# Performance work log

Hardware: AMD Instinct MI355X
Metric: run time of the kernel (lower is better)

## Reference

```python
import jax, jax.numpy as jnp
import numpy as np

B, N, D, H = 2, 4096, 512, 8
DH = D // H
FF = 4 * D
SCALE = D ** (-0.5)  # standard_scale=False -> dim**-0.5
EPS = 1e-5


def layernorm(x, w, b):
    mu = jnp.mean(x, axis=-1, keepdims=True)
    var = jnp.mean(jnp.square(x - mu), axis=-1, keepdims=True)
    return (x - mu) * jax.lax.rsqrt(var + EPS) * w + b


def setup_inputs() -> dict:
    key = jax.random.key(0)
    ks = jax.random.split(key, 12)
    s = lambda fin: 1.0 / np.sqrt(fin)
    return {
        "x": jax.random.normal(ks[0], (B, N, D), jnp.float32),
        "gamma": jax.random.uniform(ks[1], (B,), jnp.float32),
        "dist": jax.random.uniform(ks[2], (N, N), jnp.float32),
        "ln1_w": jnp.ones((D,), jnp.float32),
        "ln1_b": jnp.zeros((D,), jnp.float32),
        "qkv_w": jax.random.normal(ks[3], (D, 3 * D), jnp.float32) * s(D),
        "qkv_b": jnp.zeros((3 * D,), jnp.float32),
        "proj_w": jax.random.normal(ks[4], (D, D), jnp.float32) * s(D),
        "proj_b": jnp.zeros((D,), jnp.float32),
        "ln2_w": jnp.ones((D,), jnp.float32),
        "ln2_b": jnp.zeros((D,), jnp.float32),
        "fc1_w": jax.random.normal(ks[5], (D, FF), jnp.float32) * s(D),
        "fc1_b": jnp.zeros((FF,), jnp.float32),
        "fc2_w": jax.random.normal(ks[6], (FF, D), jnp.float32) * s(FF),
        "fc2_b": jnp.zeros((D,), jnp.float32),
    }


def reference(x, gamma, dist, ln1_w, ln1_b, qkv_w, qkv_b, proj_w, proj_b,
              ln2_w, ln2_b, fc1_w, fc1_b, fc2_w, fc2_b):
    # --- attention branch ---
    h = layernorm(x, ln1_w, ln1_b)                       # [B,N,D]
    qkv = h @ qkv_w + qkv_b                              # [B,N,3D]
    qkv = qkv.reshape(B, N, 3, H, DH).transpose(2, 0, 3, 1, 4)  # [3,B,H,N,DH]
    q, k, v = qkv[0], qkv[1], qkv[2]
    scores = jnp.einsum('bhnd,bhmd->bhnm', q, k) * SCALE
    scores = scores - gamma[:, None, None, None] * dist[None, None]
    w = jax.nn.softmax(scores, axis=-1)                  # [B,H,N,N]
    out = jnp.einsum('bhnm,bhmd->bhnd', w, v)            # [B,H,N,DH]
    out = out.transpose(0, 2, 1, 3).reshape(B, N, D)
    x = x + out @ proj_w + proj_b
    # --- MLP branch ---
    h = layernorm(x, ln2_w, ln2_b)
    h = jax.nn.gelu(h @ fc1_w + fc1_b, approximate=False)
    x = x + h @ fc2_w + fc2_b
    return x
```

## Files before the change

kernel.cpp:

```cpp
#include <hip/hip_runtime.h>
#include <math.h>

typedef __bf16 bf16x8 __attribute__((ext_vector_type(8)));
typedef __bf16 bf16x4 __attribute__((ext_vector_type(4)));
typedef float  f32x4  __attribute__((ext_vector_type(4)));
typedef unsigned int u32x4 __attribute__((ext_vector_type(4)));

#define B_   2
#define N_   4096
#define D_   512
#define H_   8
#define FF_  2048
#define BN_  (B_*N_)
static constexpr float SCALE_ = 0.04419417382415922f;
static constexpr float LOG2E_ = 1.44269504088896341f;
static constexpr float SCALE_L2E_ = SCALE_ * LOG2E_;

#define GLOAD_LDS16(g, l) __builtin_amdgcn_global_load_lds( \
    (const __attribute__((address_space(1))) void*)(g),     \
    (__attribute__((address_space(3))) void*)(l), 16, 0, 0)

__global__ void transpose_to_bf16(const float* __restrict__ in, __bf16* __restrict__ out,
                                  int R, int C) {
    __shared__ float tile[32][33];
    const int c0 = blockIdx.x * 32, r0 = blockIdx.y * 32;
    const int tx = threadIdx.x, ty = threadIdx.y;
#pragma unroll
    for (int i = 0; i < 4; ++i)
        tile[ty + 8*i][tx] = in[(size_t)(r0 + ty + 8*i) * C + c0 + tx];
    __syncthreads();
#pragma unroll
    for (int i = 0; i < 4; ++i)
        out[(size_t)(c0 + ty + 8*i) * R + r0 + tx] = (__bf16)tile[tx][ty + 8*i];
}

__global__ void cvt_bf16(const float* __restrict__ in, __bf16* __restrict__ out, int n4) {
    int i = blockIdx.x * blockDim.x + threadIdx.x;
    const int stride = gridDim.x * blockDim.x;
    for (; i < n4; i += stride) {
        float4 v = ((const float4*)in)[i];
        bf16x4 o;
        o[0] = (__bf16)(v.x * LOG2E_); o[1] = (__bf16)(v.y * LOG2E_);
        o[2] = (__bf16)(v.z * LOG2E_); o[3] = (__bf16)(v.w * LOG2E_);
        ((bf16x4*)out)[i] = o;
    }
}

__global__ __launch_bounds__(128)
void ln_kernel(const float* __restrict__ x, const float* __restrict__ w,
               const float* __restrict__ b, __bf16* __restrict__ out) {
    const int row = blockIdx.x, t = threadIdx.x;
    const float4 v = *(const float4*)&x[(size_t)row * 512 + t * 4];
    float s  = v.x + v.y + v.z + v.w;
    float sq = v.x*v.x + v.y*v.y + v.z*v.z + v.w*v.w;
#pragma unroll
    for (int mk = 1; mk < 64; mk <<= 1) { s += __shfl_xor(s, mk); sq += __shfl_xor(sq, mk); }
    __shared__ float ps[2][2];
    if ((t & 63) == 0) { ps[t >> 6][0] = s; ps[t >> 6][1] = sq; }
    __syncthreads();
    s = ps[0][0] + ps[1][0]; sq = ps[0][1] + ps[1][1];
    const float mu  = s * (1.0f / 512.0f);
    const float var = sq * (1.0f / 512.0f) - mu * mu;
    const float rs  = rsqrtf(var + 1e-5f);
    const float4 wv = *(const float4*)&w[t * 4];
    const float4 bv = *(const float4*)&b[t * 4];
    bf16x4 o;
    o[0] = (__bf16)((v.x - mu) * rs * wv.x + bv.x);
    o[1] = (__bf16)((v.y - mu) * rs * wv.y + bv.y);
    o[2] = (__bf16)((v.z - mu) * rs * wv.z + bv.z);
    o[3] = (__bf16)((v.w - mu) * rs * wv.w + bv.w);
    *(bf16x4*)&out[(size_t)row * 512 + t * 4] = o;
}

template<int EPI, int BNT, bool DBUF>
__global__ __launch_bounds__(256, 4)
void gemm_bt(const __bf16* __restrict__ A, const __bf16* __restrict__ Bt,
             const float* __restrict__ bias, const float* __restrict__ resid,
             __bf16* __restrict__ outb, float* __restrict__ outf,
             int M, int N, int K) {
    constexpr int NI = BNT / 32;
    constexpr int NB = DBUF ? 2 : 1;
    __shared__ __align__(16) __bf16 As[NB][128 * 64];
    __shared__ __align__(16) __bf16 Bs[NB][BNT * 64];
    const int tid = threadIdx.x;
    const int w = tid >> 6, l = tid & 63;
    const int g = l >> 4, c = l & 15;
    const int m0 = blockIdx.y * 128, n0 = blockIdx.x * BNT;
    const int wm = (w >> 1) * 64, wn = (w & 1) * (BNT / 2);
    f32x4 acc[4][NI] = {};

    auto stage = [&](int kt, int buf) {
#pragma unroll
        for (int i = 0; i < 4; ++i) {
            const int cb = (i * 4 + w) * 64;
            const int chunk = cb + l;
            const int row = chunk >> 3, c8 = chunk & 7;
            GLOAD_LDS16(A + (size_t)(m0 + row) * K + kt + c8 * 8, As[buf] + cb * 8);
        }
#pragma unroll
        for (int i = 0; i < BNT / 32; ++i) {
            const int cb = (i * 4 + w) * 64;
            const int chunk = cb + l;
            const int row = chunk >> 3, c8 = chunk & 7;
            GLOAD_LDS16(Bt + (size_t)(n0 + row) * K + kt + c8 * 8, Bs[buf] + cb * 8);
        }
    };
    auto compute = [&](int buf) {
#pragma unroll
        for (int kk = 0; kk < 2; ++kk) {
            bf16x8 av[4], bv[NI];
#pragma unroll
            for (int mi = 0; mi < 4; ++mi)
                av[mi] = *(const bf16x8*)&As[buf][(wm + mi * 16 + c) * 64 + kk * 32 + g * 8];
#pragma unroll
            for (int ni = 0; ni < NI; ++ni)
                bv[ni] = *(const bf16x8*)&Bs[buf][(wn + ni * 16 + c) * 64 + kk * 32 + g * 8];
#pragma unroll
            for (int mi = 0; mi < 4; ++mi)
#pragma unroll
                for (int ni = 0; ni < NI; ++ni)
                    acc[mi][ni] = __builtin_amdgcn_mfma_f32_16x16x32_bf16(
                        av[mi], bv[ni], acc[mi][ni], 0, 0, 0);
        }
    };

    if constexpr (DBUF) {
        stage(0, 0);
        const int T = K / 64;
        for (int t = 0; t < T; ++t) {
            const int cur = t & 1;
            __syncthreads();
            if (t + 1 < T) stage((t + 1) * 64, cur ^ 1);
            compute(cur);
        }
    } else {
        for (int kt = 0; kt < K; kt += 64) {
            __syncthreads();
            stage(kt, 0);
            __syncthreads();
            compute(0);
        }
    }

    __syncthreads();
    if constexpr (EPI == 2) {
        constexpr int LDW = NI * 16 + 4;
        float* ep = (float*)&As[0][0] + w * (16 * LDW);
#pragma unroll
        for (int mi = 0; mi < 4; ++mi) {
#pragma unroll
            for (int ni = 0; ni < NI; ++ni)
#pragma unroll
                for (int r = 0; r < 4; ++r)
                    ep[(g * 4 + r) * LDW + ni * 16 + c] =
                        acc[mi][ni][r] + bias[n0 + wn + ni * 16 + c];
#pragma unroll
            for (int rnd = 0; rnd < NI; ++rnd) {
                const int idx = rnd * 64 + l;
                const int rr = idx >> 3, cc = idx & 7;
                const f32x4 vv = *(const f32x4*)&ep[rr * LDW + cc * 4];
                const size_t oidx = (size_t)(m0 + wm + mi * 16 + rr) * N + n0 + wn + cc * 4;
                const f32x4 rv = *(const f32x4*)&resid[oidx];
                *(f32x4*)&outf[oidx] = vv + rv;
            }
        }
    } else {
        constexpr int LDW = NI * 16 + 8;
        __bf16* ep = &As[0][0] + w * (16 * LDW);
#pragma unroll
        for (int mi = 0; mi < 4; ++mi) {
#pragma unroll
            for (int ni = 0; ni < NI; ++ni)
#pragma unroll
                for (int r = 0; r < 4; ++r) {
                    float v = acc[mi][ni][r] + bias[n0 + wn + ni * 16 + c];
                    if constexpr (EPI == 1)
                        v = 0.5f * v * (1.0f + erff(v * 0.70710678118654752f));
                    ep[(g * 4 + r) * LDW + ni * 16 + c] = (__bf16)v;
                }
#pragma unroll
            for (int rnd = 0; rnd < NI / 2; ++rnd) {
                const int idx = rnd * 64 + l;
                const int rr = idx >> 3, cc = idx & 7;
                const bf16x8 vv = *(const bf16x8*)&ep[rr * LDW + cc * 8];
                const size_t oidx = (size_t)(m0 + wm + mi * 16 + rr) * N + n0 + wn + cc * 8;
                *(bf16x8*)&outb[oidx] = vv;
            }
        }
    }
}

__global__ __launch_bounds__(512, 4)
void attn_kernel(const __bf16* __restrict__ qkv, const __bf16* __restrict__ distb,
                 const float* __restrict__ gamma, __bf16* __restrict__ outp) {
    __shared__ __align__(16) __bf16 Ks [64 * 64];
    __shared__ __align__(16) __bf16 Vts[64][72];
    __shared__ __align__(16) __bf16 DPs[2][128 * 64];
    const int tid = threadIdx.x;
    const int w = tid >> 6, l = tid & 63;
    const int g = l >> 4, c = l & 15;
    const int wq = w & 3, hn = w >> 2;
    const int qt = blockIdx.x, h = blockIdx.y;
    const int b = blockIdx.z;
    const float gb = gamma[b];
    const size_t tok0 = (size_t)b * N_;
    const int qrow = 16 * wq + c;
    const int wub = tid & 448;
    const int srow = tid >> 3;
    const int sd0  = (tid & 7) * 8;
    const int cswz = ((tid & 7) ^ (srow & 7)) * 8;
    const int swz  = (c & 7) << 3;

    bf16x8 qf[2][2];
#pragma unroll
    for (int t = 0; t < 2; ++t) {
        const size_t qbase = (tok0 + qt * 128 + 64 * t + qrow) * 1536 + h * 64;
#pragma unroll
        for (int kk = 0; kk < 2; ++kk) {
            const bf16x8 qv = *(const bf16x8*)&qkv[qbase + kk * 32 + g * 8];
#pragma unroll
            for (int j = 0; j < 8; ++j) qf[t][kk][j] = (__bf16)((float)qv[j] * SCALE_L2E_);
        }
    }
    bf16x8 ones;
#pragma unroll
    for (int j = 0; j < 8; ++j) ones[j] = (__bf16)1.0f;

    f32x4 acc[2][4] = {};
    f32x4 accl[2] = {};
    bf16x8 vreg;

    const size_t kvstep = (size_t)64 * 1536;
    const __bf16* gk = qkv + 512  + (tok0 + srow) * 1536 + h * 64 + cswz;
    const __bf16* gv = qkv + 1024 + (tok0 + srow) * 1536 + h * 64 + sd0;
    const __bf16* gd = distb + (size_t)(qt * 128 + srow) * N_ + cswz;

    auto issue_k = [&]() {
        GLOAD_LDS16(gk, Ks + wub * 8);
        gk += kvstep;
    };
    auto issue_d = [&](int buf) {
        GLOAD_LDS16(gd,                    DPs[buf] + wub * 8);
        GLOAD_LDS16(gd + (size_t)64 * N_,  DPs[buf] + (512 + wub) * 8);
        gd += 64;
    };
    auto issue_v = [&]() {
        vreg = *(const bf16x8*)gv;
        gv += kvstep;
    };
    auto write_vts = [&]() {
        const int kp = srow ^ sd0;
#pragma unroll
        for (int j = 0; j < 8; ++j) Vts[sd0 + j][kp] = vreg[j];
    };

    const int ktend = N_ / 64;
    issue_k();
    issue_v();
    issue_d(0);

    for (int kt = 0; kt < ktend; ++kt) {
        const int cur = kt & 1;
        __syncthreads();
        write_vts();
        if (kt + 1 < ktend) {
            issue_v();
            issue_d(cur ^ 1);
        }
        __builtin_amdgcn_sched_barrier(0);

        uint32_t W[2][2][2];
#pragma unroll
        for (int nii = 0; nii < 2; ++nii) {
            const int ni = 2 * hn + nii;
            f32x4 s0, s1;
            {
                const bf16x4 dd0 = *(const bf16x4*)
                    &DPs[cur][(qrow << 6) + ((16 * ni + 4 * g) ^ swz)];
                const bf16x4 dd1 = *(const bf16x4*)
                    &DPs[cur][((64 + qrow) << 6) + ((16 * ni + 4 * g) ^ swz)];
#pragma unroll
                for (int r = 0; r < 4; ++r) {
                    s0[r] = -gb * (float)dd0[r];
                    s1[r] = -gb * (float)dd1[r];
                }
            }
            __builtin_amdgcn_s_setprio(1);
#pragma unroll
            for (int kk = 0; kk < 2; ++kk) {
                const bf16x8 kf = *(const bf16x8*)
                    &Ks[((16 * ni + c) << 6) + ((kk * 32 + g * 8) ^ swz)];
                s0 = __builtin_amdgcn_mfma_f32_16x16x32_bf16(kf, qf[0][kk], s0, 0, 0, 0);
                s1 = __builtin_amdgcn_mfma_f32_16x16x32_bf16(kf, qf[1][kk], s1, 0, 0, 0);
            }
            __builtin_amdgcn_s_setprio(0);
#pragma unroll
            for (int t = 0; t < 2; ++t) {
                const f32x4 sv = (t == 0) ? s0 : s1;
                float pv0, pv1, pv2, pv3;
                pv0 = __builtin_amdgcn_exp2f(sv[0]);
                pv1 = __builtin_amdgcn_exp2f(sv[1]);
                pv2 = __builtin_amdgcn_exp2f(sv[2]);
                pv3 = __builtin_amdgcn_exp2f(sv[3]);
                asm("v_cvt_pk_bf16_f32 %0, %1, %2" : "=v"(W[t][nii][0]) : "v"(pv0), "v"(pv1));
                asm("v_cvt_pk_bf16_f32 %0, %1, %2" : "=v"(W[t][nii][1]) : "v"(pv2), "v"(pv3));
            }
        }
        bf16x8 pa[2];
#pragma unroll
        for (int t = 0; t < 2; ++t) {
#pragma unroll
            for (int p = 0; p < 2; ++p) {
                asm("v_permlane32_swap_b32 %0, %1"
                    : "+v"(W[t][0][p]), "+v"(W[t][1][p]));
                asm("v_permlane16_swap_b32 %0, %1"
                    : "+v"(W[t][0][p]), "+v"(W[t][1][p]));
            }
            const u32x4 words = {W[t][0][0], W[t][0][1], W[t][1][0], W[t][1][1]};
            pa[t] = __builtin_bit_cast(bf16x8, words);
        }
        __builtin_amdgcn_sched_barrier(0);
        asm volatile("s_waitcnt lgkmcnt(0)\n\ts_barrier" ::: "memory");
        __builtin_amdgcn_sched_barrier(0);
        if (kt + 1 < ktend) issue_k();

        __builtin_amdgcn_s_setprio(1);
        accl[0] = __builtin_amdgcn_mfma_f32_16x16x32_bf16(ones, pa[0], accl[0], 0, 0, 0);
        accl[1] = __builtin_amdgcn_mfma_f32_16x16x32_bf16(ones, pa[1], accl[1], 0, 0, 0);
#pragma unroll
        for (int di = 0; di < 4; ++di) {
            const int d = 16 * di + c;
            const int kp = (hn * 32 + g * 8) ^ ((d >> 3) << 3);
            const bf16x8 vb = *(const bf16x8*)&Vts[d][kp];
            acc[0][di] = __builtin_amdgcn_mfma_f32_16x16x32_bf16(vb, pa[0], acc[0][di], 0, 0, 0);
            acc[1][di] = __builtin_amdgcn_mfma_f32_16x16x32_bf16(vb, pa[1], acc[1][di], 0, 0, 0);
        }
        __builtin_amdgcn_s_setprio(0);
    }

    __syncthreads();
    float* sacc = (float*)&DPs[0][0];
    float* sl   = (float*)&Ks[0];
    const int slot = wq * 64 + l;
    if (hn == 0) {
#pragma unroll
        for (int t = 0; t < 2; ++t) {
            sl[slot * 2 + t] = accl[t][0];
#pragma unroll
            for (int di = 0; di < 4; ++di)
                *(f32x4*)&sacc[(slot * 8 + t * 4 + di) * 4] = acc[t][di];
        }
    }
    __syncthreads();
    if (hn == 1) {
#pragma unroll
        for (int t = 0; t < 2; ++t) {
            const float rl = 1.0f / (accl[t][0] + sl[slot * 2 + t]);
            const int q = qt * 128 + 64 * t + qrow;
#pragma unroll
            for (int di = 0; di < 4; ++di) {
                const f32x4 oa = acc[t][di] + *(const f32x4*)&sacc[(slot * 8 + t * 4 + di) * 4];
                bf16x4 o;
#pragma unroll
                for (int r = 0; r < 4; ++r) o[r] = (__bf16)(oa[r] * rl);
                *(bf16x4*)&outp[((size_t)(b * N_ + q)) * 512 + h * 64 + 16 * di + 4 * g] = o;
            }
        }
    }
}

extern "C" void kernel_launch(void* const* d_in, const int* in_sizes, int n_in,
                              void* d_out, int out_size, void* d_ws, size_t ws_size,
                              hipStream_t stream) {
    (void)in_sizes; (void)n_in; (void)out_size; (void)ws_size;
    const float* x      = (const float*)d_in[0];
    const float* gamma  = (const float*)d_in[1];
    const float* dist   = (const float*)d_in[2];
    const float* ln1_w  = (const float*)d_in[3];
    const float* ln1_b  = (const float*)d_in[4];
    const float* qkv_w  = (const float*)d_in[5];
    const float* qkv_b  = (const float*)d_in[6];
    const float* proj_w = (const float*)d_in[7];
    const float* proj_b = (const float*)d_in[8];
    const float* ln2_w  = (const float*)d_in[9];
    const float* ln2_b  = (const float*)d_in[10];
    const float* fc1_w  = (const float*)d_in[11];
    const float* fc1_b  = (const float*)d_in[12];
    const float* fc2_w  = (const float*)d_in[13];
    const float* fc2_b  = (const float*)d_in[14];
    float* out = (float*)d_out;

    char* ws = (char*)d_ws;
    size_t off = 0;
    auto alloc = [&](size_t bytes) {
        void* p = ws + off; off = (off + bytes + 255) & ~(size_t)255; return p;
    };
    __bf16* distbf  = (__bf16*)alloc((size_t)N_ * N_ * 2);
    __bf16* qkv_wt  = (__bf16*)alloc((size_t)1536 * 512 * 2);
    __bf16* proj_wt = (__bf16*)alloc((size_t)512 * 512 * 2);
    __bf16* fc1_wt  = (__bf16*)alloc((size_t)2048 * 512 * 2);
    __bf16* fc2_wt  = (__bf16*)alloc((size_t)512 * 2048 * 2);
    __bf16* hbuf    = (__bf16*)alloc((size_t)BN_ * 512 * 2);
    __bf16* qkvbuf  = (__bf16*)alloc((size_t)BN_ * 1536 * 2);
    __bf16* attnbuf = (__bf16*)alloc((size_t)BN_ * 512 * 2);
    float*  x1buf   = (float*) alloc((size_t)BN_ * 512 * 4);
    __bf16* h2buf   = (__bf16*)alloc((size_t)BN_ * 512 * 2);
    __bf16* ffbuf   = (__bf16*)alloc((size_t)BN_ * 2048 * 2);

    const dim3 tb(32, 8);
    transpose_to_bf16<<<dim3(1536/32,  512/32), tb, 0, stream>>>(qkv_w,  qkv_wt,  512, 1536);
    transpose_to_bf16<<<dim3( 512/32,  512/32), tb, 0, stream>>>(proj_w, proj_wt, 512,  512);
    transpose_to_bf16<<<dim3(2048/32,  512/32), tb, 0, stream>>>(fc1_w,  fc1_wt,  512, 2048);
    transpose_to_bf16<<<dim3( 512/32, 2048/32), tb, 0, stream>>>(fc2_w,  fc2_wt, 2048,  512);
    cvt_bf16<<<2048, 256, 0, stream>>>(dist, distbf, N_ * N_ / 4);

    ln_kernel<<<BN_, 128, 0, stream>>>(x, ln1_w, ln1_b, hbuf);
    gemm_bt<0,128,false><<<dim3(1536/128, BN_/128), 256, 0, stream>>>(
        hbuf, qkv_wt, qkv_b, nullptr, qkvbuf, nullptr, BN_, 1536, 512);
    attn_kernel<<<dim3(32, 8, 2), 512, 0, stream>>>(qkvbuf, distbf, gamma, attnbuf);
    gemm_bt<2,64,false><<<dim3(512/64, BN_/128), 256, 0, stream>>>(
        attnbuf, proj_wt, proj_b, x, nullptr, x1buf, BN_, 512, 512);
    ln_kernel<<<BN_, 128, 0, stream>>>(x1buf, ln2_w, ln2_b, h2buf);
    gemm_bt<1,128,false><<<dim3(2048/128, BN_/128), 256, 0, stream>>>(
        h2buf, fc1_wt, fc1_b, nullptr, ffbuf, nullptr, BN_, 2048, 512);
    gemm_bt<2,64,false><<<dim3(512/64, BN_/128), 256, 0, stream>>>(
        ffbuf, fc2_wt, fc2_b, x1buf, nullptr, out, BN_, 512, 2048);
}
```

Measured before the change: 262.3 us.

## Read fp32 distance matrix directly in attention, drop bf16 conversion pre-pass

Removes the separate cvt_bf16 kernel that wrote a bf16 copy of the 4096x4096 distance matrix, so the attention kernel now streams fp32 dist tiles straight into LDS and folds log2e into gamma. The LDS dist tile becomes a single fp32 buffer instead of a double-buffered bf16 one, and its load is moved to after the mid-iteration barrier, next to the K load. This saves a full read-and-write pass over dist but doubles the dist bytes each attention block reads (32 q-tiles x 16 heads re-read it) and drops the double buffering, so dist latency may be less hidden.

```diff
diff --git a/kernel.cpp b/kernel.cpp
--- a/kernel.cpp
+++ b/kernel.cpp
@@ -32,18 +32,6 @@
 #pragma unroll
     for (int i = 0; i < 4; ++i)
         out[(size_t)(c0 + ty + 8*i) * R + r0 + tx] = (__bf16)tile[tx][ty + 8*i];
-}
-
-__global__ void cvt_bf16(const float* __restrict__ in, __bf16* __restrict__ out, int n4) {
-    int i = blockIdx.x * blockDim.x + threadIdx.x;
-    const int stride = gridDim.x * blockDim.x;
-    for (; i < n4; i += stride) {
-        float4 v = ((const float4*)in)[i];
-        bf16x4 o;
-        o[0] = (__bf16)(v.x * LOG2E_); o[1] = (__bf16)(v.y * LOG2E_);
-        o[2] = (__bf16)(v.z * LOG2E_); o[3] = (__bf16)(v.w * LOG2E_);
-        ((bf16x4*)out)[i] = o;
-    }
 }
 
 __global__ __launch_bounds__(128)
@@ -191,18 +179,18 @@
 }
 
 __global__ __launch_bounds__(512, 4)
-void attn_kernel(const __bf16* __restrict__ qkv, const __bf16* __restrict__ distb,
+void attn_kernel(const __bf16* __restrict__ qkv, const float* __restrict__ dist,
                  const float* __restrict__ gamma, __bf16* __restrict__ outp) {
     __shared__ __align__(16) __bf16 Ks [64 * 64];
     __shared__ __align__(16) __bf16 Vts[64][72];
-    __shared__ __align__(16) __bf16 DPs[2][128 * 64];
+    __shared__ __align__(16) float  DPsF[128 * 64];
     const int tid = threadIdx.x;
     const int w = tid >> 6, l = tid & 63;
     const int g = l >> 4, c = l & 15;
     const int wq = w & 3, hn = w >> 2;
     const int qt = blockIdx.x, h = blockIdx.y;
     const int b = blockIdx.z;
-    const float gb = gamma[b];
+    const float gbl = gamma[b] * LOG2E_;
     const size_t tok0 = (size_t)b * N_;
     const int qrow = 16 * wq + c;
     const int wub = tid & 448;
@@ -233,15 +221,18 @@
     const size_t kvstep = (size_t)64 * 1536;
     const __bf16* gk = qkv + 512  + (tok0 + srow) * 1536 + h * 64 + cswz;
     const __bf16* gv = qkv + 1024 + (tok0 + srow) * 1536 + h * 64 + sd0;
-    const __bf16* gd = distb + (size_t)(qt * 128 + srow) * N_ + cswz;
+    const int drow = tid >> 4;
+    const float* gd = dist + (size_t)(qt * 128 + drow) * N_
+                    + ((tid & 15) ^ (drow & 7)) * 4;
 
     auto issue_k = [&]() {
         GLOAD_LDS16(gk, Ks + wub * 8);
         gk += kvstep;
     };
-    auto issue_d = [&](int buf) {
-        GLOAD_LDS16(gd,                    DPs[buf] + wub * 8);
-        GLOAD_LDS16(gd + (size_t)64 * N_,  DPs[buf] + (512 + wub) * 8);
+    auto issue_d = [&]() {
+#pragma unroll
+        for (int i = 0; i < 4; ++i)
+            GLOAD_LDS16(gd + (size_t)i * 32 * N_, DPsF + i * 2048 + wub * 4);
         gd += 64;
     };
     auto issue_v = [&]() {
@@ -257,16 +248,12 @@
     const int ktend = N_ / 64;
     issue_k();
     issue_v();
-    issue_d(0);
+    issue_d();
 
     for (int kt = 0; kt < ktend; ++kt) {
-        const int cur = kt & 1;
         __syncthreads();
         write_vts();
-        if (kt + 1 < ktend) {
-            issue_v();
-            issue_d(cur ^ 1);
-        }
+        if (kt + 1 < ktend) issue_v();
         __builtin_amdgcn_sched_barrier(0);
 
         uint32_t W[2][2][2];
@@ -275,14 +262,13 @@
             const int ni = 2 * hn + nii;
             f32x4 s0, s1;
             {
-                const bf16x4 dd0 = *(const bf16x4*)
-                    &DPs[cur][(qrow << 6) + ((16 * ni + 4 * g) ^ swz)];
-                const bf16x4 dd1 = *(const bf16x4*)
-                    &DPs[cur][((64 + qrow) << 6) + ((16 * ni + 4 * g) ^ swz)];
+                const int dcol = (16 * ni + 4 * g) ^ ((c & 7) << 2);
+                const f32x4 dd0 = *(const f32x4*)&DPsF[(qrow << 6) + dcol];
+                const f32x4 dd1 = *(const f32x4*)&DPsF[((64 + qrow) << 6) + dcol];
 #pragma unroll
                 for (int r = 0; r < 4; ++r) {
-                    s0[r] = -gb * (float)dd0[r];
-                    s1[r] = -gb * (float)dd1[r];
+                    s0[r] = -gbl * dd0[r];
+                    s1[r] = -gbl * dd1[r];
                 }
             }
             __builtin_amdgcn_s_setprio(1);
@@ -322,7 +308,10 @@
         __builtin_amdgcn_sched_barrier(0);
         asm volatile("s_waitcnt lgkmcnt(0)\n\ts_barrier" ::: "memory");
         __builtin_amdgcn_sched_barrier(0);
-        if (kt + 1 < ktend) issue_k();
+        if (kt + 1 < ktend) {
+            issue_k();
+            issue_d();
+        }
 
         __builtin_amdgcn_s_setprio(1);
         accl[0] = __builtin_amdgcn_mfma_f32_16x16x32_bf16(ones, pa[0], accl[0], 0, 0, 0);
@@ -339,7 +328,7 @@
     }
 
     __syncthreads();
-    float* sacc = (float*)&DPs[0][0];
+    float* sacc = DPsF;
     float* sl   = (float*)&Ks[0];
     const int slot = wq * 64 + l;
     if (hn == 0) {
@@ -395,7 +384,6 @@
     auto alloc = [&](size_t bytes) {
         void* p = ws + off; off = (off + bytes + 255) & ~(size_t)255; return p;
     };
-    __bf16* distbf  = (__bf16*)alloc((size_t)N_ * N_ * 2);
     __bf16* qkv_wt  = (__bf16*)alloc((size_t)1536 * 512 * 2);
     __bf16* proj_wt = (__bf16*)alloc((size_t)512 * 512 * 2);
     __bf16* fc1_wt  = (__bf16*)alloc((size_t)2048 * 512 * 2);
@@ -412,12 +400,11 @@
     transpose_to_bf16<<<dim3( 512/32,  512/32), tb, 0, stream>>>(proj_w, proj_wt, 512,  512);
     transpose_to_bf16<<<dim3(2048/32,  512/32), tb, 0, stream>>>(fc1_w,  fc1_wt,  512, 2048);
     transpose_to_bf16<<<dim3( 512/32, 2048/32), tb, 0, stream>>>(fc2_w,  fc2_wt, 2048,  512);
-    cvt_bf16<<<2048, 256, 0, stream>>>(dist, distbf, N_ * N_ / 4);
 
     ln_kernel<<<BN_, 128, 0, stream>>>(x, ln1_w, ln1_b, hbuf);
     gemm_bt<0,128,false><<<dim3(1536/128, BN_/128), 256, 0, stream>>>(
         hbuf, qkv_wt, qkv_b, nullptr, qkvbuf, nullptr, BN_, 1536, 512);
-    attn_kernel<<<dim3(32, 8, 2), 512, 0, stream>>>(qkvbuf, distbf, gamma, attnbuf);
+    attn_kernel<<<dim3(32, 8, 2), 512, 0, stream>>>(qkvbuf, dist, gamma, attnbuf);
     gemm_bt<2,64,false><<<dim3(512/64, BN_/128), 256, 0, stream>>>(
         attnbuf, proj_wt, proj_b, x, nullptr, x1buf, BN_, 512, 512);
     ln_kernel<<<BN_, 128, 0, stream>>>(x1buf, ln2_w, ln2_b, h2buf);
```

Measured after the change: 249.3 us. 1.05x faster.
